# Kernel tuning notes

Measured on AMD Instinct MI355X. Metric: run time of the kernel, lower is better.

Reference implementation:

```python
import jax, jax.numpy as jnp
import numpy as np

FORWARD_STEPS = 300


def setup_inputs() -> dict:
    key = jax.random.key(0)
    k1, k2, k3, k4 = jax.random.split(key, 4)
    B, T, F = 1024, 2048, 16
    return {
        "vi": jax.random.uniform(k1, (B,), dtype=jnp.float32),
        "delta_y": jax.random.uniform(k2, (B,), dtype=jnp.float32),
        "v_previous": jax.random.uniform(k3, (B,), dtype=jnp.float32),
        "x_input": jax.random.uniform(k4, (B, T, F), dtype=jnp.float32),
        "w": jnp.asarray(4.1, dtype=jnp.float32),  # learned scalar, init Constant(4.1)
    }


def _newell_forward(x_input, w, forward_steps):
    B, T, F = x_input.shape
    x_last = x_input[:, -1, :]                     # [B, F]
    i_idx = jnp.arange(forward_steps, dtype=jnp.float32)  # [S]

    temps, valids = [], []
    for j in (1, 2, 3, 4):  # unrolled while_loop body, j=1..4
        d = jnp.sum(x_last[:, :j], axis=-1)        # [B]
        td = d * 150.0 / (w + x_last[:, 4 + j] * 25.0)  # [B]
        # referred_index = cast(i - td*10, int32) then clip to [0, T-1]
        ref = (i_idx[:, None] - (td * 10.0)[None, :]).astype(jnp.int32)  # [S, B]
        ref = jnp.clip(ref, 0, T - 1)
        feat = x_input[:, :, 9 + j]                # [B, T]
        temp = jnp.take_along_axis(feat, ref.T, axis=1).T  # [S, B]
        temps.append(temp)
        valids.append(jnp.any(temp != 0, axis=1))  # [S] — reduce_any over batch

    temps = jnp.stack(temps, axis=1)               # [S, 4, B]
    valid = jnp.stack(valids, axis=1)              # [S, 4]
    # early-exit semantics: ahat = temp of FIRST j with any nonzero, else zeros
    sel = jnp.argmax(valid, axis=1)                # [S]
    ahat = jnp.take_along_axis(temps, sel[:, None, None], axis=1)[:, 0, :]  # [S, B]
    ahat = jnp.where(jnp.any(valid, axis=1)[:, None], ahat, jnp.float32(0.0))
    return ahat.T                                  # [B, S] == stack(predictions, axis=1)


def reference(vi, delta_y, v_previous, x_input, w):
    return _newell_forward(x_input, w, FORWARD_STEPS)
```

## Files before the change

kernel.cpp:

```cpp
#include <hip/hip_runtime.h>

#define T_DIM 2048
#define F_DIM 16
#define B_DIM 1024
#define STEPS 300
#define BPB 4

#define OFF_VALID 16384u

__global__ void __launch_bounds__(320) kA(const float* __restrict__ x,
                                          const float* __restrict__ wptr,
                                          float* __restrict__ cbuf,
                                          unsigned long long* __restrict__ validw) {
#pragma clang fp contract(off)
    __shared__ float sF[4][STEPS];
    __shared__ float sc[4];
    int t = threadIdx.x;
    int wv = t >> 6;
    unsigned long long acc[4] = {0ull, 0ull, 0ull, 0ull};

#pragma unroll
    for (int s = 0; s < BPB; ++s) {
        int b = blockIdx.x * BPB + s;
        if (t == 0) {
            const float* xl = x + ((size_t)b * T_DIM + (T_DIM - 1)) * F_DIM;
            float w = *wptr;
            float d = 0.0f;
#pragma unroll
            for (int j0 = 0; j0 < 4; ++j0) {
                d = d + xl[j0];
                float den = w + xl[5 + j0] * 25.0f;
                float td  = (d * 150.0f) / den;
                float c   = td * 10.0f;
                sc[j0] = c;
                cbuf[j0 * B_DIM + b] = c;
            }
        }
        if (t < STEPS) {
            const float* row = x + ((size_t)b * T_DIM + t) * F_DIM;
            float2 p0 = *(const float2*)(row + 10);
            float2 p1 = *(const float2*)(row + 12);
            sF[0][t] = p0.x; sF[1][t] = p0.y; sF[2][t] = p1.x; sF[3][t] = p1.y;
        }
        __syncthreads();
        bool act = t < STEPS;
#pragma unroll
        for (int j = 0; j < 4; ++j) {
            bool bit = false;
            if (act) {
                float r = (float)t - sc[j];
                int idx = (int)r;
                idx = idx < 0 ? 0 : (idx > STEPS - 1 ? STEPS - 1 : idx);
                bit = sF[j][idx] != 0.0f;
            }
            acc[j] |= __ballot(bit);
        }
        __syncthreads();
    }
    if ((t & 63) == 0) {
#pragma unroll
        for (int j = 0; j < 4; ++j)
            if (acc[j]) atomicOr(&validw[j * 5 + wv], acc[j]);
    }
}

__global__ void __launch_bounds__(256) kC(const float* __restrict__ x,
                                          const float* __restrict__ cbuf,
                                          const unsigned long long* __restrict__ validw,
                                          float* __restrict__ out) {
#pragma clang fp contract(off)
    int g = blockIdx.x * 256 + threadIdx.x;
    if (g >= B_DIM * STEPS) return;
    int b = g / STEPS;
    int i = g - b * STEPS;
    int wi = i >> 6, bi = i & 63;
    unsigned m = 0;
#pragma unroll
    for (int j = 0; j < 4; ++j)
        m |= (unsigned)((validw[j * 5 + wi] >> bi) & 1ull) << j;
    float r = 0.0f;
    if (m) {
        int j = __ffs(m) - 1;
        float c = cbuf[j * B_DIM + b];
        float rr = (float)i - c;
        int idx = (int)rr;
        idx = idx < 0 ? 0 : (idx > STEPS - 1 ? STEPS - 1 : idx);
        r = x[((size_t)b * T_DIM + idx) * F_DIM + 10 + j];
    }
    out[g] = r;
}

extern "C" void kernel_launch(void* const* d_in, const int* in_sizes, int n_in,
                              void* d_out, int out_size, void* d_ws, size_t ws_size,
                              hipStream_t stream) {
    const float* x    = (const float*)d_in[3];
    const float* wptr = (const float*)d_in[4];
    float* out = (float*)d_out;

    float*              cbuf   = (float*)d_ws;
    unsigned long long* validw = (unsigned long long*)((char*)d_ws + OFF_VALID);

    hipMemsetAsync(validw, 0, 20 * sizeof(unsigned long long), stream);
    hipLaunchKernelGGL(kA, dim3(B_DIM / BPB), dim3(320), 0, stream, x, wptr, cbuf, validw);
    hipLaunchKernelGGL(kC, dim3((B_DIM * STEPS + 255) / 256), dim3(256), 0, stream,
                       x, cbuf, validw, out);
}
```

Measured before the change: 206.1 us.

## Use one block per batch row and gate atomics on unset valid bits

kA now processes one batch element per block (1024 blocks) instead of four sequential ones. The four cutoff values are computed by four threads in parallel rather than serially by thread 0. Each wave now issues its atomicOr only when the ballot adds bits not already present in the current global word, which is meant to cut atomic traffic. kC is reorganised so each 320-thread block handles one batch row, removing the per-thread division. The trade-off is more blocks, more per-block sync overhead, and many more racy reads of validw.

```diff
diff --git a/kernel.cpp b/kernel.cpp
--- a/kernel.cpp
+++ b/kernel.cpp
@@ -4,7 +4,6 @@
 #define F_DIM 16
 #define B_DIM 1024
 #define STEPS 300
-#define BPB 4
 
 #define OFF_VALID 16384u
 
@@ -15,65 +14,56 @@
 #pragma clang fp contract(off)
     __shared__ float sF[4][STEPS];
     __shared__ float sc[4];
+    int b = blockIdx.x;
     int t = threadIdx.x;
     int wv = t >> 6;
-    unsigned long long acc[4] = {0ull, 0ull, 0ull, 0ull};
+
+    if (t < 4) {
+        const float* xl = x + ((size_t)b * T_DIM + (T_DIM - 1)) * F_DIM;
+        float w = *wptr;
+        float d = 0.0f;
+        for (int k = 0; k <= t; ++k) d = d + xl[k];
+        float den = w + xl[5 + t] * 25.0f;
+        float td  = (d * 150.0f) / den;
+        float c   = td * 10.0f;
+        sc[t] = c;
+        cbuf[t * B_DIM + b] = c;
+    }
+    bool act = t < STEPS;
+    if (act) {
+        const float* row = x + ((size_t)b * T_DIM + t) * F_DIM;
+        float2 p0 = *(const float2*)(row + 10);
+        float2 p1 = *(const float2*)(row + 12);
+        sF[0][t] = p0.x; sF[1][t] = p0.y; sF[2][t] = p1.x; sF[3][t] = p1.y;
+    }
+    __syncthreads();
 
 #pragma unroll
-    for (int s = 0; s < BPB; ++s) {
-        int b = blockIdx.x * BPB + s;
-        if (t == 0) {
-            const float* xl = x + ((size_t)b * T_DIM + (T_DIM - 1)) * F_DIM;
-            float w = *wptr;
-            float d = 0.0f;
-#pragma unroll
-            for (int j0 = 0; j0 < 4; ++j0) {
-                d = d + xl[j0];
-                float den = w + xl[5 + j0] * 25.0f;
-                float td  = (d * 150.0f) / den;
-                float c   = td * 10.0f;
-                sc[j0] = c;
-                cbuf[j0 * B_DIM + b] = c;
-            }
+    for (int j = 0; j < 4; ++j) {
+        bool bit = false;
+        if (act) {
+            float r = (float)t - sc[j];
+            int idx = (int)r;
+            idx = idx < 0 ? 0 : (idx > STEPS - 1 ? STEPS - 1 : idx);
+            bit = sF[j][idx] != 0.0f;
         }
-        if (t < STEPS) {
-            const float* row = x + ((size_t)b * T_DIM + t) * F_DIM;
-            float2 p0 = *(const float2*)(row + 10);
-            float2 p1 = *(const float2*)(row + 12);
-            sF[0][t] = p0.x; sF[1][t] = p0.y; sF[2][t] = p1.x; sF[3][t] = p1.y;
+        unsigned long long m = __ballot(bit);
+        if ((t & 63) == 0 && m) {
+            unsigned long long cur = validw[j * 5 + wv];
+            if (m & ~cur) atomicOr(&validw[j * 5 + wv], m);
         }
-        __syncthreads();
-        bool act = t < STEPS;
-#pragma unroll
-        for (int j = 0; j < 4; ++j) {
-            bool bit = false;
-            if (act) {
-                float r = (float)t - sc[j];
-                int idx = (int)r;
-                idx = idx < 0 ? 0 : (idx > STEPS - 1 ? STEPS - 1 : idx);
-                bit = sF[j][idx] != 0.0f;
-            }
-            acc[j] |= __ballot(bit);
-        }
-        __syncthreads();
-    }
-    if ((t & 63) == 0) {
-#pragma unroll
-        for (int j = 0; j < 4; ++j)
-            if (acc[j]) atomicOr(&validw[j * 5 + wv], acc[j]);
     }
 }
 
-__global__ void __launch_bounds__(256) kC(const float* __restrict__ x,
+__global__ void __launch_bounds__(320) kC(const float* __restrict__ x,
                                           const float* __restrict__ cbuf,
                                           const unsigned long long* __restrict__ validw,
                                           float* __restrict__ out) {
 #pragma clang fp contract(off)
-    int g = blockIdx.x * 256 + threadIdx.x;
-    if (g >= B_DIM * STEPS) return;
-    int b = g / STEPS;
-    int i = g - b * STEPS;
-    int wi = i >> 6, bi = i & 63;
+    int b = blockIdx.x;
+    int t = threadIdx.x;
+    if (t >= STEPS) return;
+    int wi = t >> 6, bi = t & 63;
     unsigned m = 0;
 #pragma unroll
     for (int j = 0; j < 4; ++j)
@@ -82,12 +72,12 @@
     if (m) {
         int j = __ffs(m) - 1;
         float c = cbuf[j * B_DIM + b];
-        float rr = (float)i - c;
+        float rr = (float)t - c;
         int idx = (int)rr;
         idx = idx < 0 ? 0 : (idx > STEPS - 1 ? STEPS - 1 : idx);
         r = x[((size_t)b * T_DIM + idx) * F_DIM + 10 + j];
     }
-    out[g] = r;
+    out[b * STEPS + t] = r;
 }
 
 extern "C" void kernel_launch(void* const* d_in, const int* in_sizes, int n_in,
@@ -101,7 +91,6 @@
     unsigned long long* validw = (unsigned long long*)((char*)d_ws + OFF_VALID);
 
     hipMemsetAsync(validw, 0, 20 * sizeof(unsigned long long), stream);
-    hipLaunchKernelGGL(kA, dim3(B_DIM / BPB), dim3(320), 0, stream, x, wptr, cbuf, validw);
-    hipLaunchKernelGGL(kC, dim3((B_DIM * STEPS + 255) / 256), dim3(256), 0, stream,
-                       x, cbuf, validw, out);
+    hipLaunchKernelGGL(kA, dim3(B_DIM), dim3(320), 0, stream, x, wptr, cbuf, validw);
+    hipLaunchKernelGGL(kC, dim3(B_DIM), dim3(320), 0, stream, x, cbuf, validw, out);
 }
```

After: 281.7 us. 36.7% more time.
